# Optimization experiments

Measured on AMD Instinct MI355X. Metric: run time of the kernel, lower is better.

## Reference

```python
import jax, jax.numpy as jnp
import numpy as np

N = 50000    # nodes
E = 800000   # edges per block
D = 128      # embed_dim
H = 8        # heads
DH = D // H  # head dim
L = 2        # layers / blocks
IN = 128     # in_feats
P = 8192     # pos/neg pairs
FF = 2 * D   # FFN hidden
NEG_SLOPE = 0.2


def layer_norm(x, g, b, eps=1e-5):
    m = x.mean(-1, keepdims=True)
    v = ((x - m) ** 2).mean(-1, keepdims=True)
    return (x - m) / jnp.sqrt(v + eps) * g + b


def setup_inputs() -> dict:
    key = jax.random.key(0)
    ks = jax.random.split(key, 32)
    f32 = jnp.float32
    def w(k, shape, fan_in):
        return jax.random.normal(k, shape, f32) * (1.0 / np.sqrt(fan_in))
    inp = {
        'x': jax.random.normal(ks[0], (N, IN), f32),
        'src': jax.random.randint(ks[1], (L, E), 0, N),
        'dst': jax.random.randint(ks[2], (L, E), 0, N),
        'pos_src': jax.random.randint(ks[3], (P,), 0, N),
        'pos_dst': jax.random.randint(ks[4], (P,), 0, N),
        'neg_src': jax.random.randint(ks[5], (P,), 0, N),
        'neg_dst': jax.random.randint(ks[6], (P,), 0, N),
        # input projection
        'W_in': w(ks[7], (IN, D), IN), 'b_in': jnp.zeros((D,), f32),
        # per-layer attention weights, stacked over L
        'Wq': w(ks[8], (L, D, D), D), 'bq': jnp.zeros((L, D), f32),
        'Wk': w(ks[9], (L, D, D), D), 'bk': jnp.zeros((L, D), f32),
        'Wv': w(ks[10], (L, D, D), D), 'bv': jnp.zeros((L, D), f32),
        'Wo': w(ks[11], (L, D, D), D), 'bo': jnp.zeros((L, D), f32),
        'ln1_g': jnp.ones((L, D), f32), 'ln1_b': jnp.zeros((L, D), f32),
        'Wf1': w(ks[12], (L, D, FF), D), 'bf1': jnp.zeros((L, FF), f32),
        'Wf2': w(ks[13], (L, FF, D), FF), 'bf2': jnp.zeros((L, D), f32),
        'ln2_g': jnp.ones((L, D), f32), 'ln2_b': jnp.zeros((L, D), f32),
        # predictor MLP: D -> D//2 -> 1
        'Wp1': w(ks[14], (D, D // 2), D), 'bp1': jnp.zeros((D // 2,), f32),
        'Wp2': w(ks[15], (D // 2, 1), D // 2), 'bp2': jnp.zeros((1,), f32),
    }
    return inp


def reference(x, src, dst, pos_src, pos_dst, neg_src, neg_dst,
              W_in, b_in, Wq, bq, Wk, bk, Wv, bv, Wo, bo,
              ln1_g, ln1_b, Wf1, bf1, Wf2, bf2, ln2_g, ln2_b,
              Wp1, bp1, Wp2, bp2):
    scale = 1.0 / np.sqrt(DH)
    h = x @ W_in + b_in  # [N, D] (dropout is identity in eval mode)
    for l in range(L):
        s_l, d_l = src[l], dst[l]
        q = (h @ Wq[l] + bq[l]).reshape(N, H, DH)
        k = (h @ Wk[l] + bk[l]).reshape(N, H, DH)
        v = (h @ Wv[l] + bv[l]).reshape(N, H, DH)
        # per-edge attention scores [E, H]
        sc = jnp.einsum('ehd,ehd->eh', q[d_l], k[s_l]) * scale
        # segment softmax over incoming edges of each dst node
        m = jax.ops.segment_max(sc, d_l, num_segments=N)   # [N, H]
        ex = jnp.exp(sc - m[d_l])
        den = jax.ops.segment_sum(ex, d_l, num_segments=N)  # [N, H]
        alpha = ex / (den[d_l] + 1e-9)
        agg = jax.ops.segment_sum(alpha[..., None] * v[s_l], d_l,
                                  num_segments=N).reshape(N, D)
        h = layer_norm(h + agg @ Wo[l] + bo[l], ln1_g[l], ln1_b[l])
        ff = jax.nn.relu(h @ Wf1[l] + bf1[l]) @ Wf2[l] + bf2[l]
        h = layer_norm(h + ff, ln2_g[l], ln2_b[l])

    def predict(a, b):
        z = h[a] * h[b]  # gather-multiply edge scoring
        z = jax.nn.leaky_relu(z @ Wp1 + bp1, NEG_SLOPE)
        return z @ Wp2 + bp2  # [P, 1]

    pos_score = predict(pos_src, pos_dst)
    neg_score = predict(neg_src, neg_dst)
    return (pos_score, neg_score, h)
```

## Files before the change

kernel.cpp:

```cpp
#include <hip/hip_runtime.h>
#include <hip/hip_bf16.h>
#include <math.h>

#define N_NODES 50000
#define NE      800000
#define D       128
#define H       8
#define DH      16
#define NLAYER  2
#define IN_F    128
#define PP      8192
#define FF      256
#define MPAD    50048
#define CAP     96
#define NBIN    196
#define BCAP    48
#define GCAP    4608
#define CHUNK   2048

typedef short  bf16x8 __attribute__((ext_vector_type(8)));
typedef float  f32x4  __attribute__((ext_vector_type(4)));
typedef __hip_bfloat16 bf16;
typedef unsigned short u16;
typedef unsigned int   u32;

__device__ __forceinline__ float bflo(u32 u) { return __uint_as_float(u << 16); }
__device__ __forceinline__ float bfhi(u32 u) { return __uint_as_float(u & 0xffff0000u); }

__global__ __launch_bounds__(256) void bin_kernel(
    const int* __restrict__ dst, const int* __restrict__ src,
    u32* __restrict__ gbin, int* __restrict__ gbin_cnt)
{
    __shared__ u32 ent[NBIN * BCAP];
    __shared__ int bcnt[NBIN];
    const int t = threadIdx.x, l = blockIdx.y;
    const int base = blockIdx.x * CHUNK;
    if (t < NBIN) bcnt[t] = 0;
    __syncthreads();
    #pragma unroll
    for (int j = 0; j < CHUNK / 256; j++) {
        int e = base + j * 256 + t;
        if (e < NE) {
            int d = dst[(size_t)l * NE + e];
            int s = src[(size_t)l * NE + e];
            int bin = d >> 8;
            int slot = atomicAdd(&bcnt[bin], 1);
            if (slot < BCAP) ent[bin * BCAP + slot] = ((u32)s << 16) | (u32)(d & 255);
        }
    }
    __syncthreads();
    if (t < NBIN) {
        int c = bcnt[t]; if (c > BCAP) c = BCAP;
        if (c > 0) {
            int gb = atomicAdd(&gbin_cnt[l * NBIN + t], c);
            u32* gp = gbin + ((size_t)l * NBIN + t) * GCAP;
            for (int i = 0; i < c; i++)
                if (gb + i < GCAP) gp[gb + i] = ent[t * BCAP + i];
        }
    }
}

__global__ __launch_bounds__(256) void expand_kernel(
    const u32* __restrict__ gbin, const int* __restrict__ gbin_cnt,
    int* __restrict__ cnt, u16* __restrict__ ssrc)
{
    __shared__ int lcnt[256];
    const int t = threadIdx.x, b = blockIdx.x, l = blockIdx.y;
    lcnt[t] = 0;
    __syncthreads();
    int n = gbin_cnt[l * NBIN + b]; if (n > GCAP) n = GCAP;
    const u32* gp = gbin + ((size_t)l * NBIN + b) * GCAP;
    for (int i = t; i < n; i += 256) {
        u32 u = gp[i];
        int dl = (int)(u & 255);
        int pos = atomicAdd(&lcnt[dl], 1);
        if (pos < CAP) {
            int d = (b << 8) + dl;
            ssrc[((size_t)l * N_NODES + d) * CAP + pos] = (u16)(u >> 16);
        }
    }
    __syncthreads();
    int d = (b << 8) + t;
    if (d < N_NODES) cnt[l * N_NODES + d] = lcnt[t];
}

__global__ void xb_kernel(const float* __restrict__ x, bf16* __restrict__ xb) {
    int id = blockIdx.x * blockDim.x + threadIdx.x;
    if (id >= MPAD * IN_F) return;
    int r = id / IN_F;
    xb[id] = __float2bfloat16(r < N_NODES ? x[id] : 0.f);
}

__global__ void prep_kernel(const float* __restrict__ W_in,
                            const float* __restrict__ Wq, const float* __restrict__ Wk,
                            const float* __restrict__ Wv, const float* __restrict__ Wo,
                            const float* __restrict__ Wf1, const float* __restrict__ Wf2,
                            const float* __restrict__ bq, const float* __restrict__ bk,
                            const float* __restrict__ bv,
                            bf16* __restrict__ win_t, bf16* __restrict__ wqkv_t,
                            bf16* __restrict__ wo_t, bf16* __restrict__ wf1_t,
                            bf16* __restrict__ wf2_t, float* __restrict__ bqkv)
{
    int id = blockIdx.x * blockDim.x + threadIdx.x;
    if (id < 16384) {
        int n = id >> 7, k = id & 127;
        win_t[id] = __float2bfloat16(W_in[k * 128 + n]);
        return;
    }
    id -= 16384;
    if (id < NLAYER * 49152) {
        int l = id / 49152, j = id % 49152;
        int r = j >> 7, k = j & 127;
        const float* Ws; int col;
        if (r < 128) { Ws = Wq; col = r; }
        else {
            int u = r - 128, hh = u >> 5, w = u & 31;
            if (w < 16) { Ws = Wk; col = hh * 16 + w; }
            else        { Ws = Wv; col = hh * 16 + w - 16; }
        }
        wqkv_t[(size_t)l * 49152 + j] = __float2bfloat16(Ws[(size_t)l * 16384 + k * 128 + col]);
        return;
    }
    id -= NLAYER * 49152;
    if (id < NLAYER * 16384) {
        int l = id / 16384, j = id % 16384;
        int n = j >> 7, k = j & 127;
        wo_t[id] = __float2bfloat16(Wo[(size_t)l * 16384 + k * 128 + n]);
        return;
    }
    id -= NLAYER * 16384;
    if (id < NLAYER * 32768) {
        int l = id / 32768, j = id % 32768;
        int n = j >> 7, k = j & 127;
        wf1_t[id] = __float2bfloat16(Wf1[(size_t)l * 32768 + k * 256 + n]);
        return;
    }
    id -= NLAYER * 32768;
    if (id < NLAYER * 32768) {
        int l = id / 32768, j = id % 32768;
        int n = j >> 8, k = j & 255;
        wf2_t[id] = __float2bfloat16(Wf2[(size_t)l * 32768 + k * 128 + n]);
        return;
    }
    id -= NLAYER * 32768;
    if (id < NLAYER * 384) {
        int l = id / 384, r = id % 384;
        float v;
        if (r < 128) v = bq[l * 128 + r];
        else {
            int u = r - 128, hh = u >> 5, w = u & 31;
            v = (w < 16) ? bk[l * 128 + hh * 16 + w] : bv[l * 128 + hh * 16 + w - 16];
        }
        bqkv[l * 384 + r] = v;
    }
}

__global__ __launch_bounds__(256) void gemm_mfma(
    const bf16* __restrict__ A, const bf16* __restrict__ Wt,
    const float* __restrict__ bias,
    float* __restrict__ Cf, bf16* __restrict__ Cb,
    int Mvalid, int K, int Nc, int lda, int relu)
{
    __shared__ float4 As4[1024];
    __shared__ float4 Bs4[1024];
    char* As = (char*)As4;
    char* Bs = (char*)Bs4;
    const int t = threadIdx.x;
    const int wave = t >> 6, lane = t & 63;
    const int wr = wave >> 1, wc = wave & 1;
    const int r0 = blockIdx.x * 128, c0 = blockIdx.y * 128;

    f32x4 acc[4][4] = {};

    const int lrow   = t >> 3;
    const int lcol16 = (t & 7) * 16;

    for (int k0 = 0; k0 < K; k0 += 64) {
        #pragma unroll
        for (int p = 0; p < 4; p++) {
            int row = p * 32 + lrow;
            float4 av = *(const float4*)((const char*)(A  + (size_t)(r0 + row) * lda + k0) + lcol16);
            float4 bv = *(const float4*)((const char*)(Wt + (size_t)(c0 + row) * K + k0) + lcol16);
            int sw = lcol16 ^ ((row & 7) << 4);
            *(float4*)(As + row * 128 + sw) = av;
            *(float4*)(Bs + row * 128 + sw) = bv;
        }
        __syncthreads();
        #pragma unroll
        for (int kk = 0; kk < 2; kk++) {
            bf16x8 af[4], bfr[4];
            int kbyte = kk * 64 + (lane >> 4) * 16;
            #pragma unroll
            for (int m = 0; m < 4; m++) {
                int rowa = wr * 64 + m * 16 + (lane & 15);
                af[m]  = *(const bf16x8*)(As + rowa * 128 + (kbyte ^ ((rowa & 7) << 4)));
                int rowb = wc * 64 + m * 16 + (lane & 15);
                bfr[m] = *(const bf16x8*)(Bs + rowb * 128 + (kbyte ^ ((rowb & 7) << 4)));
            }
            #pragma unroll
            for (int m = 0; m < 4; m++)
                #pragma unroll
                for (int n = 0; n < 4; n++)
                    acc[m][n] = __builtin_amdgcn_mfma_f32_16x16x32_bf16(af[m], bfr[n], acc[m][n], 0, 0, 0);
        }
        __syncthreads();
    }

    const int colbase = c0 + wc * 64 + (lane & 15);
    const int rowbase = r0 + wr * 64 + ((lane >> 4) << 2);
    #pragma unroll
    for (int n = 0; n < 4; n++) {
        int col = colbase + n * 16;
        float bsv = bias[col];
        #pragma unroll
        for (int m = 0; m < 4; m++) {
            #pragma unroll
            for (int i = 0; i < 4; i++) {
                int row = rowbase + m * 16 + i;
                if (row < Mvalid) {
                    float v = acc[m][n][i] + bsv;
                    if (relu) v = fmaxf(v, 0.f);
                    if (Cf) Cf[(size_t)row * Nc + col] = v;
                    if (Cb) Cb[(size_t)row * Nc + col] = __float2bfloat16(v);
                }
            }
        }
    }
}

__global__ __launch_bounds__(256) void gemm_ln(
    const bf16* __restrict__ A, const bf16* __restrict__ Wt,
    const float* __restrict__ bias, const float* __restrict__ g,
    const float* __restrict__ be,
    float* __restrict__ h, bf16* __restrict__ hb,
    int K, int lda)
{
    __shared__ float4 As4[512];
    __shared__ float4 Bs4[1024];
    char* As = (char*)As4;
    char* Bs = (char*)Bs4;
    const int t = threadIdx.x;
    const int w = t >> 6, lane = t & 63;
    const int r0 = blockIdx.x * 64;

    f32x4 acc[8] = {};

    for (int k0 = 0; k0 < K; k0 += 64) {
        {
            int row = t >> 2;
            int c16 = (t & 3) * 32;
            const char* ap = (const char*)(A + (size_t)(r0 + row) * lda + k0);
            float4 a0 = *(const float4*)(ap + c16);
            float4 a1 = *(const float4*)(ap + c16 + 16);
            *(float4*)(As + row * 128 + ((c16)      ^ ((row & 7) << 4))) = a0;
            *(float4*)(As + row * 128 + ((c16 + 16) ^ ((row & 7) << 4))) = a1;
        }
        {
            int row = t >> 1;
            int c16 = (t & 1) * 64;
            const char* bp = (const char*)(Wt + (size_t)row * K + k0);
            #pragma unroll
            for (int j = 0; j < 4; j++) {
                float4 b = *(const float4*)(bp + c16 + j * 16);
                *(float4*)(Bs + row * 128 + ((c16 + j * 16) ^ ((row & 7) << 4))) = b;
            }
        }
        __syncthreads();
        #pragma unroll
        for (int kk = 0; kk < 2; kk++) {
            int kbyte = kk * 64 + (lane >> 4) * 16;
            int rowa = w * 16 + (lane & 15);
            bf16x8 af = *(const bf16x8*)(As + rowa * 128 + (kbyte ^ ((rowa & 7) << 4)));
            #pragma unroll
            for (int n = 0; n < 8; n++) {
                int rowb = n * 16 + (lane & 15);
                bf16x8 bf8 = *(const bf16x8*)(Bs + rowb * 128 + (kbyte ^ ((rowb & 7) << 4)));
                acc[n] = __builtin_amdgcn_mfma_f32_16x16x32_bf16(af, bf8, acc[n], 0, 0, 0);
            }
        }
        __syncthreads();
    }

    const int sub = lane >> 4;
    const int c   = lane & 15;
    float bsv[8], gv[8], bev[8];
    #pragma unroll
    for (int n = 0; n < 8; n++) {
        int col = n * 16 + c;
        bsv[n] = bias[col]; gv[n] = g[col]; bev[n] = be[col];
    }
    #pragma unroll
    for (int i = 0; i < 4; i++) {
        int row = r0 + w * 16 + sub * 4 + i;
        bool ok = row < N_NODES;
        float x[8];
        float s = 0.f;
        #pragma unroll
        for (int n = 0; n < 8; n++) {
            float res = ok ? h[(size_t)row * D + n * 16 + c] : 0.f;
            x[n] = res + acc[n][i] + bsv[n];
            s += x[n];
        }
        s += __shfl_xor(s, 1); s += __shfl_xor(s, 2);
        s += __shfl_xor(s, 4); s += __shfl_xor(s, 8);
        float mean = s * (1.f / 128.f);
        float v = 0.f;
        #pragma unroll
        for (int n = 0; n < 8; n++) { float dd = x[n] - mean; v += dd * dd; }
        v += __shfl_xor(v, 1); v += __shfl_xor(v, 2);
        v += __shfl_xor(v, 4); v += __shfl_xor(v, 8);
        float rstd = rsqrtf(v * (1.f / 128.f) + 1e-5f);
        if (ok) {
            #pragma unroll
            for (int n = 0; n < 8; n++) {
                float o = (x[n] - mean) * rstd * gv[n] + bev[n];
                h [(size_t)row * D + n * 16 + c] = o;
                hb[(size_t)row * D + n * 16 + c] = __float2bfloat16(o);
            }
        }
    }
}

__global__ __launch_bounds__(256) void ffn_fused(
    const bf16* __restrict__ A,
    const bf16* __restrict__ Wf1t,
    const float* __restrict__ b1,
    const bf16* __restrict__ Wf2t,
    const float* __restrict__ b2,
    const float* __restrict__ g, const float* __restrict__ be,
    float* __restrict__ h, bf16* __restrict__ hb)
{
    __shared__ char lds[81920];
    char* As = lds;
    char* Xs = lds + 16384;
    char* Bs = lds + 49152;
    const int t = threadIdx.x;
    const int w = t >> 6, lane = t & 63;
    const int r0 = blockIdx.x * 64;
    const int c = lane & 15, sub = lane >> 4;

    {
        int row = t >> 2;
        int off = (t & 3) * 64;
        const char* ap = (const char*)(A + (size_t)(r0 + row) * 128);
        #pragma unroll
        for (int j = 0; j < 4; j++) {
            float4 v = *(const float4*)(ap + off + j * 16);
            *(float4*)(As + row * 256 + ((off + j * 16) ^ ((row & 7) << 4))) = v;
        }
    }

    f32x4 acc1[16] = {};
    #pragma unroll
    for (int kc = 0; kc < 2; kc++) {
        {
            int row = t;
            const char* bp = (const char*)Wf1t + row * 256 + kc * 128;
            #pragma unroll
            for (int j = 0; j < 8; j++) {
                float4 v = *(const float4*)(bp + j * 16);
                *(float4*)(Bs + row * 128 + ((j * 16) ^ ((row & 7) << 4))) = v;
            }
        }
        __syncthreads();
        #pragma unroll
        for (int kkl = 0; kkl < 2; kkl++) {
            int abyte = (kc * 2 + kkl) * 64 + sub * 16;
            int rowa = w * 16 + c;
            bf16x8 af = *(const bf16x8*)(As + rowa * 256 + (abyte ^ ((rowa & 7) << 4)));
            int bbyte = kkl * 64 + sub * 16;
            #pragma unroll
            for (int n = 0; n < 16; n++) {
                int rowb = n * 16 + c;
                bf16x8 bf8 = *(const bf16x8*)(Bs + rowb * 128 + (bbyte ^ ((rowb & 7) << 4)));
                acc1[n] = __builtin_amdgcn_mfma_f32_16x16x32_bf16(af, bf8, acc1[n], 0, 0, 0);
            }
        }
        __syncthreads();
    }

    #pragma unroll
    for (int n = 0; n < 16; n++) {
        float bs = b1[n * 16 + c];
        #pragma unroll
        for (int i = 0; i < 4; i++) {
            int row = w * 16 + sub * 4 + i;
            float v = fmaxf(acc1[n][i] + bs, 0.f);
            int byte = (n * 16 + c) * 2;
            int addr = row * 512 + ((byte & ~15) ^ ((row & 7) << 4)) + (byte & 15);
            *(bf16*)(Xs + addr) = __float2bfloat16(v);
        }
    }
    __syncthreads();

    f32x4 acc2[8] = {};
    #pragma unroll
    for (int kc = 0; kc < 2; kc++) {
        {
            int row = t >> 1;
            int off = (t & 1) * 128;
            const char* bp = (const char*)Wf2t + row * 512 + kc * 256 + off;
            #pragma unroll
            for (int j = 0; j < 8; j++) {
                float4 v = *(const float4*)(bp + j * 16);
                *(float4*)(Bs + row * 256 + ((off + j * 16) ^ ((row & 7) << 4))) = v;
            }
        }
        __syncthreads();
        #pragma unroll
        for (int kkl = 0; kkl < 4; kkl++) {
            int xbyte = kc * 256 + kkl * 64 + sub * 16;
            int rowa = w * 16 + c;
            bf16x8 af = *(const bf16x8*)(Xs + rowa * 512 + (xbyte ^ ((rowa & 7) << 4)));
            int bbyte = kkl * 64 + sub * 16;
            #pragma unroll
            for (int n = 0; n < 8; n++) {
                int rowb = n * 16 + c;
                bf16x8 bf8 = *(const bf16x8*)(Bs + rowb * 256 + (bbyte ^ ((rowb & 7) << 4)));
                acc2[n] = __builtin_amdgcn_mfma_f32_16x16x32_bf16(af, bf8, acc2[n], 0, 0, 0);
            }
        }
        __syncthreads();
    }

    float bsv[8], gv[8], bev[8];
    #pragma unroll
    for (int n = 0; n < 8; n++) {
        int col = n * 16 + c;
        bsv[n] = b2[col]; gv[n] = g[col]; bev[n] = be[col];
    }
    #pragma unroll
    for (int i = 0; i < 4; i++) {
        int row = r0 + w * 16 + sub * 4 + i;
        bool ok = row < N_NODES;
        float x[8];
        float s = 0.f;
        #pragma unroll
        for (int n = 0; n < 8; n++) {
            float res = ok ? h[(size_t)row * D + n * 16 + c] : 0.f;
            x[n] = res + acc2[n][i] + bsv[n];
            s += x[n];
        }
        s += __shfl_xor(s, 1); s += __shfl_xor(s, 2);
        s += __shfl_xor(s, 4); s += __shfl_xor(s, 8);
        float mean = s * (1.f / 128.f);
        float v = 0.f;
        #pragma unroll
        for (int n = 0; n < 8; n++) { float dd = x[n] - mean; v += dd * dd; }
        v += __shfl_xor(v, 1); v += __shfl_xor(v, 2);
        v += __shfl_xor(v, 4); v += __shfl_xor(v, 8);
        float rstd = rsqrtf(v * (1.f / 128.f) + 1e-5f);
        if (ok) {
            #pragma unroll
            for (int n = 0; n < 8; n++) {
                float o = (x[n] - mean) * rstd * gv[n] + bev[n];
                h [(size_t)row * D + n * 16 + c] = o;
                hb[(size_t)row * D + n * 16 + c] = __float2bfloat16(o);
            }
        }
    }
}

__global__ __launch_bounds__(256) void attn_fused(
    const bf16* __restrict__ qkv,
    const int* __restrict__ cnt, const u16* __restrict__ ssrc,
    bf16* __restrict__ aggout)
{
    const float S2 = 0.25f * 1.44269504088896f;
    int wid = threadIdx.x >> 6, lane = threadIdx.x & 63;
    int d = blockIdx.x * 4 + wid;
    if (d >= N_NODES) return;
    int slot = lane >> 3, h = lane & 7;

    const u32* qr = (const u32*)(qkv + (size_t)d * 384 + h * DH);
    float qf[16];
    {
        uint4 q0 = *(const uint4*)(qr);
        uint4 q1 = *(const uint4*)(qr + 4);
        qf[0]=bflo(q0.x); qf[1]=bfhi(q0.x); qf[2]=bflo(q0.y); qf[3]=bfhi(q0.y);
        qf[4]=bflo(q0.z); qf[5]=bfhi(q0.z); qf[6]=bflo(q0.w); qf[7]=bfhi(q0.w);
        qf[8]=bflo(q1.x); qf[9]=bfhi(q1.x); qf[10]=bflo(q1.y); qf[11]=bfhi(q1.y);
        qf[12]=bflo(q1.z); qf[13]=bfhi(q1.z); qf[14]=bflo(q1.w); qf[15]=bfhi(q1.w);
    }

    int deg = cnt[d];
    if (deg > CAP) deg = CAP;
    const u16* bp = ssrc + (size_t)d * CAP;
    float m2 = -INFINITY, den = 0.f;
    float acc[16] = {};

    for (int i = slot; i < deg; i += 8) {
        int s = bp[i];
        const uint4* kvp = (const uint4*)(qkv + (size_t)s * 384 + 128 + h * 32);
        uint4 k0 = kvp[0], k1 = kvp[1], v0 = kvp[2], v1 = kvp[3];
        float p = qf[0]*bflo(k0.x) + qf[1]*bfhi(k0.x)
                + qf[2]*bflo(k0.y) + qf[3]*bfhi(k0.y)
                + qf[4]*bflo(k0.z) + qf[5]*bfhi(k0.z)
                + qf[6]*bflo(k0.w) + qf[7]*bfhi(k0.w)
                + qf[8]*bflo(k1.x) + qf[9]*bfhi(k1.x)
                + qf[10]*bflo(k1.y) + qf[11]*bfhi(k1.y)
                + qf[12]*bflo(k1.z) + qf[13]*bfhi(k1.z)
                + qf[14]*bflo(k1.w) + qf[15]*bfhi(k1.w);
        float p2 = p * S2;
        float w;
        if (p2 > m2 + 8.f) {
            float f = exp2f(m2 - p2);
            den *= f;
            #pragma unroll
            for (int j = 0; j < 16; j++) acc[j] *= f;
            m2 = p2;
            w = 1.f;
        } else {
            w = exp2f(p2 - m2);
        }
        den += w;
        acc[0]  += w*bflo(v0.x); acc[1]  += w*bfhi(v0.x);
        acc[2]  += w*bflo(v0.y); acc[3]  += w*bfhi(v0.y);
        acc[4]  += w*bflo(v0.z); acc[5]  += w*bfhi(v0.z);
        acc[6]  += w*bflo(v0.w); acc[7]  += w*bfhi(v0.w);
        acc[8]  += w*bflo(v1.x); acc[9]  += w*bfhi(v1.x);
        acc[10] += w*bflo(v1.y); acc[11] += w*bfhi(v1.y);
        acc[12] += w*bflo(v1.z); acc[13] += w*bfhi(v1.z);
        acc[14] += w*bflo(v1.w); acc[15] += w*bfhi(v1.w);
    }

    #pragma unroll
    for (int o = 8; o < 64; o <<= 1) {
        float om   = __shfl_xor(m2, o);
        float oden = __shfl_xor(den, o);
        float M = fmaxf(m2, om);
        float fa = (m2 > -INFINITY) ? exp2f(m2 - M) : 0.f;
        float fb = (om > -INFINITY) ? exp2f(om - M) : 0.f;
        den = den * fa + oden * fb;
        #pragma unroll
        for (int j = 0; j < 16; j++) {
            float oa = __shfl_xor(acc[j], o);
            acc[j] = acc[j] * fa + oa * fb;
        }
        m2 = M;
    }

    float r = 1.f / (den + 1e-9f);
    float o0 = 0.f, o1 = 0.f;
    #pragma unroll
    for (int j = 0; j < 8; j++) {
        if (slot == j) { o0 = acc[2 * j]; o1 = acc[2 * j + 1]; }
    }
    bf16* op = aggout + (size_t)d * 384 + h * DH + slot * 2;
    op[0] = __float2bfloat16(o0 * r);
    op[1] = __float2bfloat16(o1 * r);
}

__global__ void predict_kernel(const float* __restrict__ h,
                               const int* __restrict__ ps, const int* __restrict__ pd,
                               const int* __restrict__ ns, const int* __restrict__ nd,
                               const float* __restrict__ Wp1, const float* __restrict__ bp1,
                               const float* __restrict__ Wp2, const float* __restrict__ bp2,
                               float* __restrict__ out)
{
    __shared__ float z[128];
    int p = blockIdx.x;
    int a, b;
    if (p < PP) { a = ps[p]; b = pd[p]; }
    else        { a = ns[p - PP]; b = nd[p - PP]; }
    int t = threadIdx.x;
    z[t]      = h[(size_t)a * D + t]      * h[(size_t)b * D + t];
    z[t + 64] = h[(size_t)a * D + t + 64] * h[(size_t)b * D + t + 64];
    __syncthreads();
    float acc = bp1[t];
    #pragma unroll 4
    for (int i = 0; i < 128; i++) acc += z[i] * Wp1[(size_t)i * 64 + t];
    acc = acc > 0.f ? acc : 0.2f * acc;
    float part = acc * Wp2[t];
    #pragma unroll
    for (int o = 32; o > 0; o >>= 1) part += __shfl_down(part, o);
    if (t == 0) out[p] = part + bp2[0];
}

extern "C" void kernel_launch(void* const* d_in, const int* in_sizes, int n_in,
                              void* d_out, int out_size, void* d_ws, size_t ws_size,
                              hipStream_t stream)
{
    const float* x       = (const float*)d_in[0];
    const int*   src     = (const int*)d_in[1];
    const int*   dst     = (const int*)d_in[2];
    const int*   pos_src = (const int*)d_in[3];
    const int*   pos_dst = (const int*)d_in[4];
    const int*   neg_src = (const int*)d_in[5];
    const int*   neg_dst = (const int*)d_in[6];
    const float* W_in = (const float*)d_in[7];
    const float* b_in = (const float*)d_in[8];
    const float* Wq = (const float*)d_in[9];
    const float* bq = (const float*)d_in[10];
    const float* Wk = (const float*)d_in[11];
    const float* bk = (const float*)d_in[12];
    const float* Wv = (const float*)d_in[13];
    const float* bv = (const float*)d_in[14];
    const float* Wo = (const float*)d_in[15];
    const float* bo = (const float*)d_in[16];
    const float* ln1g = (const float*)d_in[17];
    const float* ln1b = (const float*)d_in[18];
    const float* Wf1 = (const float*)d_in[19];
    const float* bf1 = (const float*)d_in[20];
    const float* Wf2 = (const float*)d_in[21];
    const float* bf2 = (const float*)d_in[22];
    const float* ln2g = (const float*)d_in[23];
    const float* ln2b = (const float*)d_in[24];
    const float* Wp1 = (const float*)d_in[25];
    const float* bp1 = (const float*)d_in[26];
    const float* Wp2 = (const float*)d_in[27];
    const float* bp2 = (const float*)d_in[28];

    float* out = (float*)d_out;
    float* h   = out + 2 * PP;

    bf16* B    = (bf16*)d_ws;
    bf16* qkvb = B;
    bf16* xb   = B;
    bf16* hb   = B + (size_t)MPAD * 384;
    int*  cnt  = (int*)(hb + (size_t)MPAD * 128);
    u16*  ssrc = (u16*)(cnt + 2 * N_NODES);
    bf16* wtb  = (bf16*)(ssrc + (size_t)2 * N_NODES * CAP);
    bf16* win_t  = wtb;
    bf16* wqkv_t = wtb + 16384;
    bf16* wo_t   = wtb + 16384 + 98304;
    bf16* wf1_t  = wtb + 16384 + 98304 + 32768;
    bf16* wf2_t  = wtb + 16384 + 98304 + 32768 + 65536;
    float* bqkv  = (float*)(wtb + 16384 + 98304 + 32768 + 65536 + 65536);
    int*  gbin_cnt = (int*)(bqkv + NLAYER * 384);
    u32*  gbin     = (u32*)(gbin_cnt + 2 * NBIN);

    auto cdiv = [](int a, int b) { return (a + b - 1) / b; };
    const int GX = MPAD / 128;
    const int GL = MPAD / 64;

    xb_kernel<<<cdiv(MPAD * IN_F, 256), 256, 0, stream>>>(x, xb);
    prep_kernel<<<1091, 256, 0, stream>>>(W_in, Wq, Wk, Wv, Wo, Wf1, Wf2, bq, bk, bv,
                                          win_t, wqkv_t, wo_t, wf1_t, wf2_t, bqkv);

    (void)hipMemsetAsync(gbin_cnt, 0, 2 * NBIN * sizeof(int), stream);
    bin_kernel<<<dim3(cdiv(NE, CHUNK), 2), 256, 0, stream>>>(dst, src, gbin, gbin_cnt);
    expand_kernel<<<dim3(NBIN, 2), 256, 0, stream>>>(gbin, gbin_cnt, cnt, ssrc);

    gemm_mfma<<<dim3(GX, 1), 256, 0, stream>>>(xb, win_t, b_in, h, hb, N_NODES, 128, 128, 128, 0);

    for (int l = 0; l < NLAYER; l++) {
        gemm_mfma<<<dim3(GX, 3), 256, 0, stream>>>(hb, wqkv_t + l * 49152, bqkv + l * 384,
                                                   nullptr, qkvb, N_NODES, 128, 384, 128, 0);

        attn_fused<<<cdiv(N_NODES, 4), 256, 0, stream>>>(qkvb, cnt + l * N_NODES,
                                                         ssrc + (size_t)l * N_NODES * CAP, qkvb);

        gemm_ln<<<GL, 256, 0, stream>>>(qkvb, wo_t + l * 16384, bo + l * D,
                                        ln1g + l * D, ln1b + l * D, h, hb, 128, 384);

        ffn_fused<<<GL, 256, 0, stream>>>(hb, wf1_t + l * 32768, bf1 + l * FF,
                                          wf2_t + l * 32768, bf2 + l * D,
                                          ln2g + l * D, ln2b + l * D, h, hb);
    }

    predict_kernel<<<2 * PP, 64, 0, stream>>>(h, pos_src, pos_dst, neg_src, neg_dst,
                                              Wp1, bp1, Wp2, bp2, out);
}
```

Measured before the change: 377.8 us.

## Fuse output projection LayerNorm with FFN into one tail kernel

Merges the Wo GEMM + residual + LayerNorm kernel with the FFN + LayerNorm kernel. The intermediate normalized activations stay in registers (fp32, for the second residual) and in LDS (bf16, as the FFN input), instead of being written to and reread from global memory. This removes one launch per layer and a large intermediate round trip through HBM. The cost is higher register pressure from keeping the post-LN1 values live across both FFN GEMMs, which may reduce occupancy.

New measurement: 362.0 us. 1.04x faster.

```diff
diff --git a/kernel.cpp b/kernel.cpp
--- a/kernel.cpp
+++ b/kernel.cpp
@@ -228,127 +228,107 @@
     }
 }
 
-__global__ __launch_bounds__(256) void gemm_ln(
-    const bf16* __restrict__ A, const bf16* __restrict__ Wt,
-    const float* __restrict__ bias, const float* __restrict__ g,
-    const float* __restrict__ be,
-    float* __restrict__ h, bf16* __restrict__ hb,
-    int K, int lda)
-{
-    __shared__ float4 As4[512];
-    __shared__ float4 Bs4[1024];
-    char* As = (char*)As4;
-    char* Bs = (char*)Bs4;
-    const int t = threadIdx.x;
-    const int w = t >> 6, lane = t & 63;
-    const int r0 = blockIdx.x * 64;
-
-    f32x4 acc[8] = {};
-
-    for (int k0 = 0; k0 < K; k0 += 64) {
-        {
-            int row = t >> 2;
-            int c16 = (t & 3) * 32;
-            const char* ap = (const char*)(A + (size_t)(r0 + row) * lda + k0);
-            float4 a0 = *(const float4*)(ap + c16);
-            float4 a1 = *(const float4*)(ap + c16 + 16);
-            *(float4*)(As + row * 128 + ((c16)      ^ ((row & 7) << 4))) = a0;
-            *(float4*)(As + row * 128 + ((c16 + 16) ^ ((row & 7) << 4))) = a1;
-        }
-        {
-            int row = t >> 1;
-            int c16 = (t & 1) * 64;
-            const char* bp = (const char*)(Wt + (size_t)row * K + k0);
-            #pragma unroll
-            for (int j = 0; j < 4; j++) {
-                float4 b = *(const float4*)(bp + c16 + j * 16);
-                *(float4*)(Bs + row * 128 + ((c16 + j * 16) ^ ((row & 7) << 4))) = b;
-            }
-        }
-        __syncthreads();
-        #pragma unroll
-        for (int kk = 0; kk < 2; kk++) {
-            int kbyte = kk * 64 + (lane >> 4) * 16;
-            int rowa = w * 16 + (lane & 15);
-            bf16x8 af = *(const bf16x8*)(As + rowa * 128 + (kbyte ^ ((rowa & 7) << 4)));
-            #pragma unroll
-            for (int n = 0; n < 8; n++) {
-                int rowb = n * 16 + (lane & 15);
-                bf16x8 bf8 = *(const bf16x8*)(Bs + rowb * 128 + (kbyte ^ ((rowb & 7) << 4)));
-                acc[n] = __builtin_amdgcn_mfma_f32_16x16x32_bf16(af, bf8, acc[n], 0, 0, 0);
-            }
-        }
-        __syncthreads();
-    }
-
-    const int sub = lane >> 4;
-    const int c   = lane & 15;
-    float bsv[8], gv[8], bev[8];
-    #pragma unroll
-    for (int n = 0; n < 8; n++) {
-        int col = n * 16 + c;
-        bsv[n] = bias[col]; gv[n] = g[col]; bev[n] = be[col];
-    }
-    #pragma unroll
-    for (int i = 0; i < 4; i++) {
-        int row = r0 + w * 16 + sub * 4 + i;
-        bool ok = row < N_NODES;
-        float x[8];
-        float s = 0.f;
-        #pragma unroll
-        for (int n = 0; n < 8; n++) {
-            float res = ok ? h[(size_t)row * D + n * 16 + c] : 0.f;
-            x[n] = res + acc[n][i] + bsv[n];
-            s += x[n];
-        }
-        s += __shfl_xor(s, 1); s += __shfl_xor(s, 2);
-        s += __shfl_xor(s, 4); s += __shfl_xor(s, 8);
-        float mean = s * (1.f / 128.f);
-        float v = 0.f;
-        #pragma unroll
-        for (int n = 0; n < 8; n++) { float dd = x[n] - mean; v += dd * dd; }
-        v += __shfl_xor(v, 1); v += __shfl_xor(v, 2);
-        v += __shfl_xor(v, 4); v += __shfl_xor(v, 8);
-        float rstd = rsqrtf(v * (1.f / 128.f) + 1e-5f);
-        if (ok) {
-            #pragma unroll
-            for (int n = 0; n < 8; n++) {
-                float o = (x[n] - mean) * rstd * gv[n] + bev[n];
-                h [(size_t)row * D + n * 16 + c] = o;
-                hb[(size_t)row * D + n * 16 + c] = __float2bfloat16(o);
-            }
-        }
-    }
-}
-
-__global__ __launch_bounds__(256) void ffn_fused(
-    const bf16* __restrict__ A,
+__global__ __launch_bounds__(256) void tail_fused(
+    const bf16* __restrict__ qkv,
+    const bf16* __restrict__ wo_t,
+    const float* __restrict__ bo,
+    const float* __restrict__ g1, const float* __restrict__ be1,
     const bf16* __restrict__ Wf1t,
     const float* __restrict__ b1,
     const bf16* __restrict__ Wf2t,
     const float* __restrict__ b2,
-    const float* __restrict__ g, const float* __restrict__ be,
+    const float* __restrict__ g2, const float* __restrict__ be2,
     float* __restrict__ h, bf16* __restrict__ hb)
 {
     __shared__ char lds[81920];
-    char* As = lds;
-    char* Xs = lds + 16384;
-    char* Bs = lds + 49152;
+    char* AsA = lds;
+    char* Ah1 = lds;
+    char* Xs  = lds + 16384;
+    char* Bs  = lds + 49152;
     const int t = threadIdx.x;
     const int w = t >> 6, lane = t & 63;
     const int r0 = blockIdx.x * 64;
     const int c = lane & 15, sub = lane >> 4;
 
+    f32x4 acc0[8] = {};
+    #pragma unroll
+    for (int k0 = 0; k0 < 128; k0 += 64) {
+        {
+            int row = t >> 2;
+            int c16 = (t & 3) * 32;
+            const char* ap = (const char*)(qkv + (size_t)(r0 + row) * 384 + k0);
+            float4 a0 = *(const float4*)(ap + c16);
+            float4 a1 = *(const float4*)(ap + c16 + 16);
+            *(float4*)(AsA + row * 128 + ((c16)      ^ ((row & 7) << 4))) = a0;
+            *(float4*)(AsA + row * 128 + ((c16 + 16) ^ ((row & 7) << 4))) = a1;
+        }
+        {
+            int row = t >> 1;
+            int c16 = (t & 1) * 64;
+            const char* bp = (const char*)(wo_t + (size_t)row * 128 + k0);
+            #pragma unroll
+            for (int j = 0; j < 4; j++) {
+                float4 b = *(const float4*)(bp + c16 + j * 16);
+                *(float4*)(Bs + row * 128 + ((c16 + j * 16) ^ ((row & 7) << 4))) = b;
+            }
+        }
+        __syncthreads();
+        #pragma unroll
+        for (int kk = 0; kk < 2; kk++) {
+            int kbyte = kk * 64 + sub * 16;
+            int rowa = w * 16 + c;
+            bf16x8 af = *(const bf16x8*)(AsA + rowa * 128 + (kbyte ^ ((rowa & 7) << 4)));
+            #pragma unroll
+            for (int n = 0; n < 8; n++) {
+                int rowb = n * 16 + c;
+                bf16x8 bf8 = *(const bf16x8*)(Bs + rowb * 128 + (kbyte ^ ((rowb & 7) << 4)));
+                acc0[n] = __builtin_amdgcn_mfma_f32_16x16x32_bf16(af, bf8, acc0[n], 0, 0, 0);
+            }
+        }
+        __syncthreads();
+    }
+
+    float h1v[8][4];
     {
-        int row = t >> 2;
-        int off = (t & 3) * 64;
-        const char* ap = (const char*)(A + (size_t)(r0 + row) * 128);
-        #pragma unroll
-        for (int j = 0; j < 4; j++) {
-            float4 v = *(const float4*)(ap + off + j * 16);
-            *(float4*)(As + row * 256 + ((off + j * 16) ^ ((row & 7) << 4))) = v;
-        }
-    }
+        float bsv[8], gv[8], bev[8];
+        #pragma unroll
+        for (int n = 0; n < 8; n++) {
+            int col = n * 16 + c;
+            bsv[n] = bo[col]; gv[n] = g1[col]; bev[n] = be1[col];
+        }
+        #pragma unroll
+        for (int i = 0; i < 4; i++) {
+            int row = r0 + w * 16 + sub * 4 + i;
+            bool ok = row < N_NODES;
+            float x[8];
+            float s = 0.f;
+            #pragma unroll
+            for (int n = 0; n < 8; n++) {
+                float res = ok ? h[(size_t)row * D + n * 16 + c] : 0.f;
+                x[n] = res + acc0[n][i] + bsv[n];
+                s += x[n];
+            }
+            s += __shfl_xor(s, 1); s += __shfl_xor(s, 2);
+            s += __shfl_xor(s, 4); s += __shfl_xor(s, 8);
+            float mean = s * (1.f / 128.f);
+            float v = 0.f;
+            #pragma unroll
+            for (int n = 0; n < 8; n++) { float dd = x[n] - mean; v += dd * dd; }
+            v += __shfl_xor(v, 1); v += __shfl_xor(v, 2);
+            v += __shfl_xor(v, 4); v += __shfl_xor(v, 8);
+            float rstd = rsqrtf(v * (1.f / 128.f) + 1e-5f);
+            int lrow = w * 16 + sub * 4 + i;
+            #pragma unroll
+            for (int n = 0; n < 8; n++) {
+                float o = (x[n] - mean) * rstd * gv[n] + bev[n];
+                h1v[n][i] = o;
+                int byte = (n * 16 + c) * 2;
+                int addr = lrow * 256 + ((byte & ~15) ^ ((lrow & 7) << 4)) + (byte & 15);
+                *(bf16*)(Ah1 + addr) = __float2bfloat16(o);
+            }
+        }
+    }
+    __syncthreads();
 
     f32x4 acc1[16] = {};
     #pragma unroll
@@ -367,7 +347,7 @@
         for (int kkl = 0; kkl < 2; kkl++) {
             int abyte = (kc * 2 + kkl) * 64 + sub * 16;
             int rowa = w * 16 + c;
-            bf16x8 af = *(const bf16x8*)(As + rowa * 256 + (abyte ^ ((rowa & 7) << 4)));
+            bf16x8 af = *(const bf16x8*)(Ah1 + rowa * 256 + (abyte ^ ((rowa & 7) << 4)));
             int bbyte = kkl * 64 + sub * 16;
             #pragma unroll
             for (int n = 0; n < 16; n++) {
@@ -423,39 +403,40 @@
         __syncthreads();
     }
 
-    float bsv[8], gv[8], bev[8];
-    #pragma unroll
-    for (int n = 0; n < 8; n++) {
-        int col = n * 16 + c;
-        bsv[n] = b2[col]; gv[n] = g[col]; bev[n] = be[col];
-    }
-    #pragma unroll
-    for (int i = 0; i < 4; i++) {
-        int row = r0 + w * 16 + sub * 4 + i;
-        bool ok = row < N_NODES;
-        float x[8];
-        float s = 0.f;
+    {
+        float bsv[8], gv[8], bev[8];
         #pragma unroll
         for (int n = 0; n < 8; n++) {
-            float res = ok ? h[(size_t)row * D + n * 16 + c] : 0.f;
-            x[n] = res + acc2[n][i] + bsv[n];
-            s += x[n];
-        }
-        s += __shfl_xor(s, 1); s += __shfl_xor(s, 2);
-        s += __shfl_xor(s, 4); s += __shfl_xor(s, 8);
-        float mean = s * (1.f / 128.f);
-        float v = 0.f;
-        #pragma unroll
-        for (int n = 0; n < 8; n++) { float dd = x[n] - mean; v += dd * dd; }
-        v += __shfl_xor(v, 1); v += __shfl_xor(v, 2);
-        v += __shfl_xor(v, 4); v += __shfl_xor(v, 8);
-        float rstd = rsqrtf(v * (1.f / 128.f) + 1e-5f);
-        if (ok) {
+            int col = n * 16 + c;
+            bsv[n] = b2[col]; gv[n] = g2[col]; bev[n] = be2[col];
+        }
+        #pragma unroll
+        for (int i = 0; i < 4; i++) {
+            int row = r0 + w * 16 + sub * 4 + i;
+            bool ok = row < N_NODES;
+            float x[8];
+            float s = 0.f;
             #pragma unroll
             for (int n = 0; n < 8; n++) {
-                float o = (x[n] - mean) * rstd * gv[n] + bev[n];
-                h [(size_t)row * D + n * 16 + c] = o;
-                hb[(size_t)row * D + n * 16 + c] = __float2bfloat16(o);
+                x[n] = h1v[n][i] + acc2[n][i] + bsv[n];
+                s += x[n];
+            }
+            s += __shfl_xor(s, 1); s += __shfl_xor(s, 2);
+            s += __shfl_xor(s, 4); s += __shfl_xor(s, 8);
+            float mean = s * (1.f / 128.f);
+            float v = 0.f;
+            #pragma unroll
+            for (int n = 0; n < 8; n++) { float dd = x[n] - mean; v += dd * dd; }
+            v += __shfl_xor(v, 1); v += __shfl_xor(v, 2);
+            v += __shfl_xor(v, 4); v += __shfl_xor(v, 8);
+            float rstd = rsqrtf(v * (1.f / 128.f) + 1e-5f);
+            if (ok) {
+                #pragma unroll
+                for (int n = 0; n < 8; n++) {
+                    float o = (x[n] - mean) * rstd * gv[n] + bev[n];
+                    h [(size_t)row * D + n * 16 + c] = o;
+                    hb[(size_t)row * D + n * 16 + c] = __float2bfloat16(o);
+                }
             }
         }
     }
@@ -651,12 +632,11 @@
         attn_fused<<<cdiv(N_NODES, 4), 256, 0, stream>>>(qkvb, cnt + l * N_NODES,
                                                          ssrc + (size_t)l * N_NODES * CAP, qkvb);
 
-        gemm_ln<<<GL, 256, 0, stream>>>(qkvb, wo_t + l * 16384, bo + l * D,
-                                        ln1g + l * D, ln1b + l * D, h, hb, 128, 384);
-
-        ffn_fused<<<GL, 256, 0, stream>>>(hb, wf1_t + l * 32768, bf1 + l * FF,
-                                          wf2_t + l * 32768, bf2 + l * D,
-                                          ln2g + l * D, ln2b + l * D, h, hb);
+        tail_fused<<<GL, 256, 0, stream>>>(qkvb, wo_t + l * 16384, bo + l * D,
+                                           ln1g + l * D, ln1b + l * D,
+                                           wf1_t + l * 32768, bf1 + l * FF,
+                                           wf2_t + l * 32768, bf2 + l * D,
+                                           ln2g + l * D, ln2b + l * D, h, hb);
     }
 
     predict_kernel<<<2 * PP, 64, 0, stream>>>(h, pos_src, pos_dst, neg_src, neg_dst,
```
